# Kernel tuning notes

Hardware: AMD Instinct MI355X
Metric: run time of the kernel (lower is better)

## Reference

```python
import jax, jax.numpy as jnp
import numpy as np

EMB = 2048
HEADS = 16
HEAD = EMB // HEADS


def setup_inputs() -> dict:
    key = jax.random.key(0)
    ks = jax.random.split(key, 10)
    B, S = 4, 2048
    x = jax.random.normal(ks[0], (B, S, EMB), dtype=jnp.float32)
    # additive causal mask: 0 on/below diagonal, -inf above
    neg_inf = jnp.finfo(jnp.float32).min
    attn_mask = jnp.where(jnp.tril(jnp.ones((S, S), dtype=bool)), 0.0, neg_inf).astype(jnp.float32)
    scale = 1.0 / np.sqrt(EMB)  # xavier-ish init scale
    Wq = jax.random.normal(ks[1], (EMB, EMB), dtype=jnp.float32) * scale
    Wk = jax.random.normal(ks[2], (EMB, EMB), dtype=jnp.float32) * scale
    Wv = jax.random.normal(ks[3], (EMB, EMB), dtype=jnp.float32) * scale
    Wo = jax.random.normal(ks[4], (EMB, EMB), dtype=jnp.float32) * scale
    bq = jnp.zeros((EMB,), dtype=jnp.float32)
    bk = jnp.zeros((EMB,), dtype=jnp.float32)
    bv = jnp.zeros((EMB,), dtype=jnp.float32)
    bo = jnp.zeros((EMB,), dtype=jnp.float32)
    return {"x": x, "attn_mask": attn_mask, "Wq": Wq, "bq": bq, "Wk": Wk, "bk": bk,
            "Wv": Wv, "bv": bv, "Wo": Wo, "bo": bo}


def reference(x, attn_mask, Wq, bq, Wk, bk, Wv, bv, Wo, bo):
    B, S, E = x.shape
    # torch Linear: y = x @ W.T + b
    def proj(W, b):
        y = jnp.einsum('bse,fe->bsf', x, W) + b
        return y.reshape(B, S, HEADS, HEAD).transpose(0, 2, 1, 3)  # [B,H,S,D]
    q = proj(Wq, bq)
    k = proj(Wk, bk)
    v = proj(Wv, bv)
    scores = jnp.einsum('bhqd,bhkd->bhqk', q, k) / np.sqrt(HEAD)
    scores = scores + attn_mask  # broadcast [S,S] over [B,H,S,S]
    attn = jax.nn.softmax(scores, axis=-1)  # dropout p=0.0 -> identity
    ctx = jnp.einsum('bhqk,bhkd->bhqd', attn, v)
    ctx = ctx.transpose(0, 2, 1, 3).reshape(B, S, E)
    out = jnp.einsum('bse,fe->bsf', ctx, Wo) + bo
    return out
```

## Files before the change

kernel.cpp:

```cpp
#include <hip/hip_runtime.h>

#define BATCH 4
#define SEQ   2048
#define EMBD  2048
#define NHEAD 16
#define HEADD 128

#define GM (BATCH*SEQ)
#define GN EMBD
#define GK EMBD

typedef __attribute__((ext_vector_type(8))) short short8;
typedef __attribute__((ext_vector_type(4))) short s16x4;
typedef __attribute__((ext_vector_type(4))) float f32x4;

static __device__ __forceinline__ short f2bf(float f) {
  unsigned u = __builtin_bit_cast(unsigned, f);
  unsigned r = (u + 0x7fffu + ((u >> 16) & 1u)) >> 16;
  return (short)r;
}

static __device__ __forceinline__ unsigned cvt_pk_bf16(float lo, float hi) {
  unsigned r;
  asm("v_cvt_pk_bf16_f32 %0, %1, %2" : "=v"(r) : "v"(lo), "v"(hi));
  return r;
}

static __device__ __forceinline__ void glds16(const short* g, short* l) {
  __builtin_amdgcn_global_load_lds(
      (const __attribute__((address_space(1))) unsigned int*)g,
      (__attribute__((address_space(3))) unsigned int*)l, 16, 0, 0);
}

__global__ __launch_bounds__(256) void cvt_f32_bf16(
    const float* __restrict__ in, short* __restrict__ out, int n)
{
  int i = (blockIdx.x * 256 + threadIdx.x) * 8;
  if (i + 7 < n) {
    float4 a = *(const float4*)&in[i];
    float4 b = *(const float4*)&in[i + 4];
    short8 o;
    o[0] = f2bf(a.x); o[1] = f2bf(a.y); o[2] = f2bf(a.z); o[3] = f2bf(a.w);
    o[4] = f2bf(b.x); o[5] = f2bf(b.y); o[6] = f2bf(b.z); o[7] = f2bf(b.w);
    *(short8*)&out[i] = o;
  }
}

__global__ __launch_bounds__(256) void cvt_w4(
    const float* __restrict__ w0, const float* __restrict__ w1,
    const float* __restrict__ w2, const float* __restrict__ w3,
    short* __restrict__ o0, short* __restrict__ o1,
    short* __restrict__ o2, short* __restrict__ o3)
{
  const float* src = blockIdx.y == 0 ? w0 : blockIdx.y == 1 ? w1 : blockIdx.y == 2 ? w2 : w3;
  short*       dst = blockIdx.y == 0 ? o0 : blockIdx.y == 1 ? o1 : blockIdx.y == 2 ? o2 : o3;
  int i = (blockIdx.x * 256 + threadIdx.x) * 8;
  float4 a = *(const float4*)&src[i];
  float4 b = *(const float4*)&src[i + 4];
  short8 o;
  o[0] = f2bf(a.x); o[1] = f2bf(a.y); o[2] = f2bf(a.z); o[3] = f2bf(a.w);
  o[4] = f2bf(b.x); o[5] = f2bf(b.y); o[6] = f2bf(b.z); o[7] = f2bf(b.w);
  *(short8*)&dst[i] = o;
}

#define NKT (GK / 64)

template<bool F32OUT>
__global__ __launch_bounds__(512, 2) void gemm_bias_kernel(
    const short* __restrict__ A, const short* __restrict__ W,
    const float* __restrict__ bias, void* __restrict__ Cout)
{
  __shared__ short SH[2][2][2][128 * 64];

  const int tid  = threadIdx.x;
  const int lane = tid & 63;
  const int wv   = tid >> 6;
  const int quad = lane >> 4;
  const int l15  = lane & 15;
  const int rsw  = l15 & 7;

  const int bid = blockIdx.x;
  const int swz = (bid & 7) * 32 + (bid >> 3);
  const int n0 = (swz & 7) * 256;
  const int m0 = (swz >> 3) * 256;

  const int hA = wv >> 2;
  const int hB = (wv & 3) >> 1;
  const int bl = (wv & 1) * 64;

  int grow[2], gcol[2];
#pragma unroll
  for (int j = 0; j < 2; ++j) {
    int gi = j * 512 + tid;
    int row = gi >> 3, slot = gi & 7;
    grow[j] = row;
    gcol[j] = (slot ^ (row & 7)) * 8;
  }

#define STG(mat_, src_, rb_, kt_, h_) do {                                   \
    short* ld_ = &SH[(kt_) & 1][mat_][h_][0];                                \
    _Pragma("unroll")                                                        \
    for (int j = 0; j < 2; ++j)                                              \
      glds16(&src_[(size_t)((rb_) + (h_) * 128 + grow[j]) * GK +             \
                   (kt_) * 64 + gcol[j]],                                    \
             &ld_[(j * 512 + wv * 64) * 8]);                                 \
  } while (0)

#define ARD(mi_, ks_) (*(const short8*)&Abase[                               \
    (((mi_) * 16 + l15) * 8 + (((ks_) * 4 + quad) ^ rsw)) * 8])
#define BRD(ni_, ks_) (*(const short8*)&Bbase[                               \
    ((bl + (ni_) * 16 + l15) * 8 + (((ks_) * 4 + quad) ^ rsw)) * 8])

  const f32x4 zerov = {0.f, 0.f, 0.f, 0.f};
  f32x4 acc[8][4];
#pragma unroll
  for (int mi = 0; mi < 8; ++mi)
#pragma unroll
    for (int ni = 0; ni < 4; ++ni) acc[mi][ni] = zerov;

  STG(0, A, m0, 0, 0); STG(1, W, n0, 0, 0); STG(1, W, n0, 0, 1);
  STG(0, A, m0, 0, 1);
  STG(1, W, n0, 1, 0); STG(1, W, n0, 1, 1); STG(0, A, m0, 1, 0);
  asm volatile("s_waitcnt vmcnt(6)" ::: "memory");
  __builtin_amdgcn_sched_barrier(0);
  __builtin_amdgcn_s_barrier();

  for (int kt = 0; kt < NKT; ++kt) {
    const int d = kt & 1;
    const short* Abase = &SH[d][0][hA][0];
    const short* Bbase = &SH[d][1][hB][0];
    short8 afA[4][2], afB[4][2], bfA[2][2], bfB[2][2];

#pragma unroll
    for (int mi = 0; mi < 4; ++mi)
#pragma unroll
      for (int ks = 0; ks < 2; ++ks) afA[mi][ks] = ARD(mi, ks);
#pragma unroll
    for (int ni = 0; ni < 2; ++ni)
#pragma unroll
      for (int ks = 0; ks < 2; ++ks) bfA[ni][ks] = BRD(ni, ks);
    if (kt + 1 < NKT) STG(0, A, m0, kt + 1, 1);
    __builtin_amdgcn_sched_barrier(0);
    asm volatile("s_waitcnt lgkmcnt(8)" ::: "memory");
    __builtin_amdgcn_s_barrier();
    asm volatile("s_waitcnt lgkmcnt(0)" ::: "memory");
    __builtin_amdgcn_sched_barrier(0);
    __builtin_amdgcn_s_setprio(1);
#pragma unroll
    for (int mi = 0; mi < 4; ++mi)
#pragma unroll
      for (int ni = 0; ni < 2; ++ni)
#pragma unroll
        for (int ks = 0; ks < 2; ++ks)
          acc[mi][ni] = __builtin_amdgcn_mfma_f32_16x16x32_bf16(afA[mi][ks], bfA[ni][ks], acc[mi][ni], 0, 0, 0);
    __builtin_amdgcn_s_setprio(0);
    __builtin_amdgcn_sched_barrier(0);
    __builtin_amdgcn_s_barrier();

#pragma unroll
    for (int ni = 0; ni < 2; ++ni)
#pragma unroll
      for (int ks = 0; ks < 2; ++ks) bfB[ni][ks] = BRD(ni + 2, ks);
    __builtin_amdgcn_sched_barrier(0);
    __builtin_amdgcn_s_barrier();
    asm volatile("s_waitcnt lgkmcnt(0)" ::: "memory");
    __builtin_amdgcn_sched_barrier(0);
    __builtin_amdgcn_s_setprio(1);
#pragma unroll
    for (int mi = 0; mi < 4; ++mi)
#pragma unroll
      for (int ni = 0; ni < 2; ++ni)
#pragma unroll
        for (int ks = 0; ks < 2; ++ks)
          acc[mi][ni + 2] = __builtin_amdgcn_mfma_f32_16x16x32_bf16(afA[mi][ks], bfB[ni][ks], acc[mi][ni + 2], 0, 0, 0);
    __builtin_amdgcn_s_setprio(0);
    __builtin_amdgcn_sched_barrier(0);
    __builtin_amdgcn_s_barrier();

#pragma unroll
    for (int mi = 0; mi < 4; ++mi)
#pragma unroll
      for (int ks = 0; ks < 2; ++ks) afB[mi][ks] = ARD(mi + 4, ks);
    if (kt + 2 < NKT) STG(1, W, n0, kt + 2, 0);
    __builtin_amdgcn_sched_barrier(0);
    __builtin_amdgcn_s_barrier();
    asm volatile("s_waitcnt lgkmcnt(0)" ::: "memory");
    __builtin_amdgcn_sched_barrier(0);
    __builtin_amdgcn_s_setprio(1);
#pragma unroll
    for (int mi = 0; mi < 4; ++mi)
#pragma unroll
      for (int ni = 0; ni < 2; ++ni)
#pragma unroll
        for (int ks = 0; ks < 2; ++ks)
          acc[mi + 4][ni] = __builtin_amdgcn_mfma_f32_16x16x32_bf16(afB[mi][ks], bfA[ni][ks], acc[mi + 4][ni], 0, 0, 0);
    __builtin_amdgcn_s_setprio(0);
    __builtin_amdgcn_sched_barrier(0);
    __builtin_amdgcn_s_barrier();

    if (kt + 2 < NKT) { STG(1, W, n0, kt + 2, 1); STG(0, A, m0, kt + 2, 0); }
    if (kt + 2 < NKT)      asm volatile("s_waitcnt vmcnt(6)" ::: "memory");
    else if (kt + 1 < NKT) asm volatile("s_waitcnt vmcnt(0)" ::: "memory");
    __builtin_amdgcn_sched_barrier(0);
    __builtin_amdgcn_s_barrier();
    __builtin_amdgcn_sched_barrier(0);
    __builtin_amdgcn_s_setprio(1);
#pragma unroll
    for (int mi = 0; mi < 4; ++mi)
#pragma unroll
      for (int ni = 0; ni < 2; ++ni)
#pragma unroll
        for (int ks = 0; ks < 2; ++ks)
          acc[mi + 4][ni + 2] = __builtin_amdgcn_mfma_f32_16x16x32_bf16(afB[mi][ks], bfB[ni][ks], acc[mi + 4][ni + 2], 0, 0, 0);
    __builtin_amdgcn_s_setprio(0);
    __builtin_amdgcn_sched_barrier(0);
    __builtin_amdgcn_s_barrier();
  }
#undef STG
#undef ARD
#undef BRD

  const int wm0 = hA * 128;
  const int wn0 = (wv & 3) * 64;
#pragma unroll
  for (int mi = 0; mi < 8; ++mi) {
    int mg = m0 + wm0 + mi * 16 + quad * 4;
#pragma unroll
    for (int ni = 0; ni < 4; ++ni) {
      int ng = n0 + wn0 + ni * 16 + l15;
      float bv = bias[ng];
#pragma unroll
      for (int r = 0; r < 4; ++r) {
        float val = acc[mi][ni][r] + bv;
        if (F32OUT)
          ((float*)Cout)[(size_t)(mg + r) * GN + ng] = val;
        else
          ((short*)Cout)[(size_t)(mg + r) * GN + ng] = f2bf(val);
      }
    }
  }
}

__global__ __launch_bounds__(256) void transpose_v(
    const short* __restrict__ V, short* __restrict__ Vt)
{
  __shared__ short T[64][72];
  const int b  = blockIdx.z;
  const int n0 = blockIdx.x * 64;
  const int s0 = blockIdx.y * 64;
#pragma unroll
  for (int rr = 0; rr < 2; ++rr) {
    int c = rr * 256 + threadIdx.x;
    int srow = c >> 3;
    int ncol = (c & 7) << 3;
    *(short8*)&T[srow][ncol] = *(const short8*)&V[((size_t)b * SEQ + s0 + srow) * EMBD + n0 + ncol];
  }
  __syncthreads();
#pragma unroll
  for (int rr = 0; rr < 2; ++rr) {
    int c = rr * 256 + threadIdx.x;
    int nrow = c >> 3;
    int scol = (c & 7) << 3;
    short8 o;
#pragma unroll
    for (int j = 0; j < 8; ++j) o[j] = T[scol + j][nrow];
    *(short8*)&Vt[((size_t)b * EMBD + n0 + nrow) * SEQ + s0 + scol] = o;
  }
}

__global__ __launch_bounds__(256) void flash_attn(
    const short* __restrict__ Q, const short* __restrict__ K,
    const short* __restrict__ Vt, short* __restrict__ Ctx)
{
  __shared__ short Ksf[2][64 * 128];
  __shared__ short Vsf[2][128 * 64];
  __shared__ short Ps[4][16][72];

  const int bid  = blockIdx.x;
  const int slot = bid >> 3;
  const int grp  = ((bid & 7) << 3) | (slot >> 4);
  const int xq   = slot & 15;
  const int h = grp & 15, b = grp >> 4;

  const int tid = threadIdx.x, lane = tid & 63, wv = tid >> 6;
  const int quad = lane >> 4, l15 = lane & 15;

  const size_t bhq    = (size_t)b * SEQ * EMBD + (size_t)h * HEADD;
  const size_t vtbase = ((size_t)b * EMBD + (size_t)h * HEADD) * SEQ;
  const float SL2E = 0.08838834764831845f * 1.4426950408889634f;
  const float THRS = 8.0f / SL2E;
  const int NQT = SEQ / 64;

  int kco[4], koff[4], voff[4];
#pragma unroll
  for (int rr = 0; rr < 4; ++rr) {
    int c = rr * 4 + wv;
    int g = c * 64 + lane;
    kco[rr] = c * 512;
    { int row = g >> 4, col16 = (g & 15) ^ (row & 15);
      koff[rr] = row * EMBD + col16 * 8; }
    { int row = g >> 3, col8 = (g & 7) ^ (row & 7);
      voff[rr] = row * SEQ + col8 * 8; }
  }

#define STAGE(buf, kt_) do {                                                 \
    const short* kb_ = &K[bhq + (size_t)((kt_) * 64) * EMBD];                \
    const short* vb_ = &Vt[vtbase + (size_t)((kt_) * 64)];                   \
    _Pragma("unroll")                                                        \
    for (int rr = 0; rr < 4; ++rr) {                                         \
      glds16(&kb_[koff[rr]], &Ksf[buf][kco[rr]]);                            \
      glds16(&vb_[voff[rr]], &Vsf[buf][kco[rr]]);                            \
    }                                                                        \
  } while (0)

  const f32x4 zerov = {0.f, 0.f, 0.f, 0.f};

  for (int pass = 0; pass < 2; ++pass) {
    const int qt = pass ? (NQT - 1 - xq) : xq;
    const int qg    = qt * 64 + wv * 16 + l15;
    const int rowg0 = qt * 64 + wv * 16 + quad * 4;

    short8 qf[4];
#pragma unroll
    for (int ks = 0; ks < 4; ++ks)
      qf[ks] = *(const short8*)&Q[bhq + (size_t)qg * EMBD + ks * 32 + quad * 8];

    f32x4 oacc[8];
#pragma unroll
    for (int ni = 0; ni < 8; ++ni) oacc[ni] = zerov;
    float m_s = -INFINITY;
    float l_s = 0.f;

    __syncthreads();
    STAGE(0, 0);

    for (int kt = 0; kt <= qt; ++kt) {
      const int cur = kt & 1;
      __syncthreads();
      if (kt < qt) STAGE(cur ^ 1, kt + 1);

      f32x4 sA[4];
#pragma unroll
      for (int ni = 0; ni < 4; ++ni) sA[ni] = zerov;
#pragma unroll
      for (int ks = 0; ks < 4; ++ks)
#pragma unroll
        for (int ni = 0; ni < 4; ++ni) {
          int row = ni * 16 + l15;
          short8 kf = *(const short8*)&Ksf[cur][(row * 16 + ((ks * 4 + quad) ^ (row & 15))) * 8];
          sA[ni] = __builtin_amdgcn_mfma_f32_16x16x32_bf16(kf, qf[ks], sA[ni], 0, 0, 0);
        }

      if (kt == qt) {
        const int key00 = kt * 64;
#pragma unroll
        for (int ni = 0; ni < 4; ++ni)
#pragma unroll
          for (int r = 0; r < 4; ++r) {
            int keyg = key00 + ni * 16 + quad * 4 + r;
            if (keyg > qg) sA[ni][r] = -INFINITY;
          }
      }

      float mv = sA[0][0];
#pragma unroll
      for (int ni = 0; ni < 4; ++ni)
#pragma unroll
        for (int r = 0; r < 4; ++r)
          if (ni | r) mv = fmaxf(mv, sA[ni][r]);
      mv = fmaxf(mv, __shfl_xor(mv, 16, 64));
      mv = fmaxf(mv, __shfl_xor(mv, 32, 64));

      if (!__all(mv <= m_s + THRS)) {
        float mn = fmaxf(m_s, mv);
        float alpha = exp2f((m_s - mn) * SL2E);
        m_s = mn;
        l_s *= alpha;
        float al[4];
#pragma unroll
        for (int r = 0; r < 4; ++r) al[r] = __shfl(alpha, quad * 4 + r, 16);
#pragma unroll
        for (int ni = 0; ni < 8; ++ni)
#pragma unroll
          for (int r = 0; r < 4; ++r) oacc[ni][r] *= al[r];
      }

      float msl = m_s * SL2E;
      float sum = 0.f;
#pragma unroll
      for (int ni = 0; ni < 4; ++ni)
#pragma unroll
        for (int r = 0; r < 4; ++r) {
          float p = exp2f(sA[ni][r] * SL2E - msl);
          sA[ni][r] = p;
          sum += p;
        }
      sum += __shfl_xor(sum, 16, 64);
      sum += __shfl_xor(sum, 32, 64);
      l_s += sum;

#pragma unroll
      for (int ni = 0; ni < 4; ++ni) {
        uint2 pk;
        pk.x = cvt_pk_bf16(sA[ni][0], sA[ni][1]);
        pk.y = cvt_pk_bf16(sA[ni][2], sA[ni][3]);
        *(uint2*)&Ps[wv][l15][ni * 16 + quad * 4] = pk;
      }

      short8 pf[2];
#pragma unroll
      for (int ks = 0; ks < 2; ++ks)
        pf[ks] = *(const short8*)&Ps[wv][l15][ks * 32 + quad * 8];
#pragma unroll
      for (int ni = 0; ni < 8; ++ni)
#pragma unroll
        for (int ks = 0; ks < 2; ++ks) {
          int row = ni * 16 + l15;
          short8 vf = *(const short8*)&Vsf[cur][(row * 8 + ((ks * 4 + quad) ^ (row & 7))) * 8];
          oacc[ni] = __builtin_amdgcn_mfma_f32_16x16x32_bf16(pf[ks], vf, oacc[ni], 0, 0, 0);
        }
    }

    float linv = 1.0f / l_s;
    float iv[4];
#pragma unroll
    for (int r = 0; r < 4; ++r) iv[r] = __shfl(linv, quad * 4 + r, 16);
#pragma unroll
    for (int r = 0; r < 4; ++r)
#pragma unroll
      for (int ni = 0; ni < 8; ++ni)
        Ctx[bhq + (size_t)(rowg0 + r) * EMBD + ni * 16 + l15] = f2bf(oacc[ni][r] * iv[r]);
  }
#undef STAGE
}

extern "C" void kernel_launch(void* const* d_in, const int* in_sizes, int n_in,
                              void* d_out, int out_size, void* d_ws, size_t ws_size,
                              hipStream_t stream)
{
  const float* x  = (const float*)d_in[0];
  const float* Wq = (const float*)d_in[2];
  const float* bq = (const float*)d_in[3];
  const float* Wk = (const float*)d_in[4];
  const float* bk = (const float*)d_in[5];
  const float* Wv = (const float*)d_in[6];
  const float* bv = (const float*)d_in[7];
  const float* Wo = (const float*)d_in[8];
  const float* bo = (const float*)d_in[9];
  float* out = (float*)d_out;

  const size_t NE = (size_t)BATCH * SEQ * EMBD;
  const size_t NW = (size_t)EMBD * EMBD;
  short* xb  = (short*)d_ws;
  short* wqb = xb  + NE;
  short* wkb = wqb + NW;
  short* wvb = wkb + NW;
  short* wob = wvb + NW;
  short* q   = wob + NW;
  short* k   = q   + NE;
  short* v   = k   + NE;
  short* vt  = v   + NE;
  short* ctx = v;

  cvt_f32_bf16<<<NE / (256 * 8), 256, 0, stream>>>(x, xb, (int)NE);
  cvt_w4<<<dim3(NW / (256 * 8), 4), 256, 0, stream>>>(Wq, Wk, Wv, Wo, wqb, wkb, wvb, wob);

  dim3 gg((GM / 256) * (GN / 256));
  gemm_bias_kernel<false><<<gg, 512, 0, stream>>>(xb, wqb, bq, q);
  gemm_bias_kernel<false><<<gg, 512, 0, stream>>>(xb, wkb, bk, k);
  gemm_bias_kernel<false><<<gg, 512, 0, stream>>>(xb, wvb, bv, v);
  transpose_v<<<dim3(EMBD / 64, SEQ / 64, BATCH), 256, 0, stream>>>(v, vt);
  flash_attn<<<dim3((SEQ / 128) * NHEAD * BATCH), 256, 0, stream>>>(q, k, vt, ctx);
  gemm_bias_kernel<true><<<gg, 512, 0, stream>>>(ctx, wob, bo, out);
}
```

Before: 571.5 us.

## Enlarge flash-attention query tile to 128 rows with 8 waves per block

Raises the flash-attention block from 4 to 8 waves, each block now covering 128 query rows, so every staged K/V tile is reused by twice as many waves and the grid shrinks to 512 blocks with a new block-to-head mapping. It also swizzles the P scratch buffer in LDS to avoid bank conflicts, adds scheduling barriers around the async staging, and raises wave priority around the MFMA loops. The trade-offs are fewer blocks in the grid for load balancing, higher register pressure under the new launch bounds, and more diagonal-tile masking work per block.

```diff
diff --git a/kernel.cpp b/kernel.cpp
--- a/kernel.cpp
+++ b/kernel.cpp
@@ -268,18 +268,17 @@
   }
 }
 
-__global__ __launch_bounds__(256) void flash_attn(
+__global__ __launch_bounds__(512, 4) void flash_attn(
     const short* __restrict__ Q, const short* __restrict__ K,
     const short* __restrict__ Vt, short* __restrict__ Ctx)
 {
   __shared__ short Ksf[2][64 * 128];
   __shared__ short Vsf[2][128 * 64];
-  __shared__ short Ps[4][16][72];
-
-  const int bid  = blockIdx.x;
-  const int slot = bid >> 3;
-  const int grp  = ((bid & 7) << 3) | (slot >> 4);
-  const int xq   = slot & 15;
+  __shared__ short Ps[8][16 * 64];
+
+  const int bid = blockIdx.x;
+  const int grp = ((bid & 7) << 3) | (bid >> 6);
+  const int xq  = (bid >> 3) & 7;
   const int h = grp & 15, b = grp >> 4;
 
   const int tid = threadIdx.x, lane = tid & 63, wv = tid >> 6;
@@ -289,12 +288,12 @@
   const size_t vtbase = ((size_t)b * EMBD + (size_t)h * HEADD) * SEQ;
   const float SL2E = 0.08838834764831845f * 1.4426950408889634f;
   const float THRS = 8.0f / SL2E;
-  const int NQT = SEQ / 64;
-
-  int kco[4], koff[4], voff[4];
-#pragma unroll
-  for (int rr = 0; rr < 4; ++rr) {
-    int c = rr * 4 + wv;
+  const int NQT = SEQ / 128;
+
+  int kco[2], koff[2], voff[2];
+#pragma unroll
+  for (int rr = 0; rr < 2; ++rr) {
+    int c = rr * 8 + wv;
     int g = c * 64 + lane;
     kco[rr] = c * 512;
     { int row = g >> 4, col16 = (g & 15) ^ (row & 15);
@@ -307,7 +306,7 @@
     const short* kb_ = &K[bhq + (size_t)((kt_) * 64) * EMBD];                \
     const short* vb_ = &Vt[vtbase + (size_t)((kt_) * 64)];                   \
     _Pragma("unroll")                                                        \
-    for (int rr = 0; rr < 4; ++rr) {                                         \
+    for (int rr = 0; rr < 2; ++rr) {                                         \
       glds16(&kb_[koff[rr]], &Ksf[buf][kco[rr]]);                            \
       glds16(&vb_[voff[rr]], &Vsf[buf][kco[rr]]);                            \
     }                                                                        \
@@ -317,8 +316,9 @@
 
   for (int pass = 0; pass < 2; ++pass) {
     const int qt = pass ? (NQT - 1 - xq) : xq;
-    const int qg    = qt * 64 + wv * 16 + l15;
-    const int rowg0 = qt * 64 + wv * 16 + quad * 4;
+    const int qg    = qt * 128 + wv * 16 + l15;
+    const int rowg0 = qt * 128 + wv * 16 + quad * 4;
+    const int KTMAX = 2 * qt + 1;
 
     short8 qf[4];
 #pragma unroll
@@ -332,16 +332,21 @@
     float l_s = 0.f;
 
     __syncthreads();
+    __builtin_amdgcn_sched_barrier(0);
     STAGE(0, 0);
-
-    for (int kt = 0; kt <= qt; ++kt) {
+    __builtin_amdgcn_sched_barrier(0);
+
+    for (int kt = 0; kt <= KTMAX; ++kt) {
       const int cur = kt & 1;
       __syncthreads();
-      if (kt < qt) STAGE(cur ^ 1, kt + 1);
+      __builtin_amdgcn_sched_barrier(0);
+      if (kt < KTMAX) STAGE(cur ^ 1, kt + 1);
+      __builtin_amdgcn_sched_barrier(0);
 
       f32x4 sA[4];
 #pragma unroll
       for (int ni = 0; ni < 4; ++ni) sA[ni] = zerov;
+      __builtin_amdgcn_s_setprio(1);
 #pragma unroll
       for (int ks = 0; ks < 4; ++ks)
 #pragma unroll
@@ -350,8 +355,9 @@
           short8 kf = *(const short8*)&Ksf[cur][(row * 16 + ((ks * 4 + quad) ^ (row & 15))) * 8];
           sA[ni] = __builtin_amdgcn_mfma_f32_16x16x32_bf16(kf, qf[ks], sA[ni], 0, 0, 0);
         }
-
-      if (kt == qt) {
+      __builtin_amdgcn_s_setprio(0);
+
+      if (kt >= 2 * qt) {
         const int key00 = kt * 64;
 #pragma unroll
         for (int ni = 0; ni < 4; ++ni)
@@ -404,13 +410,16 @@
         uint2 pk;
         pk.x = cvt_pk_bf16(sA[ni][0], sA[ni][1]);
         pk.y = cvt_pk_bf16(sA[ni][2], sA[ni][3]);
-        *(uint2*)&Ps[wv][l15][ni * 16 + quad * 4] = pk;
+        int wg = (((ni * 2 + (quad >> 1)) ^ (l15 & 7)) << 3) + ((quad & 1) << 2);
+        *(uint2*)&Ps[wv][l15 * 64 + wg] = pk;
       }
 
       short8 pf[2];
 #pragma unroll
       for (int ks = 0; ks < 2; ++ks)
-        pf[ks] = *(const short8*)&Ps[wv][l15][ks * 32 + quad * 8];
+        pf[ks] = *(const short8*)&Ps[wv][l15 * 64 + (((ks * 4 + quad) ^ (l15 & 7)) << 3)];
+
+      __builtin_amdgcn_s_setprio(1);
 #pragma unroll
       for (int ni = 0; ni < 8; ++ni)
 #pragma unroll
@@ -419,6 +428,8 @@
           short8 vf = *(const short8*)&Vsf[cur][(row * 8 + ((ks * 4 + quad) ^ (row & 7))) * 8];
           oacc[ni] = __builtin_amdgcn_mfma_f32_16x16x32_bf16(pf[ks], vf, oacc[ni], 0, 0, 0);
         }
+      __builtin_amdgcn_s_setprio(0);
+      __builtin_amdgcn_sched_barrier(0);
     }
 
     float linv = 1.0f / l_s;
@@ -470,6 +481,6 @@
   gemm_bias_kernel<false><<<gg, 512, 0, stream>>>(xb, wkb, bk, k);
   gemm_bias_kernel<false><<<gg, 512, 0, stream>>>(xb, wvb, bv, v);
   transpose_v<<<dim3(EMBD / 64, SEQ / 64, BATCH), 256, 0, stream>>>(v, vt);
-  flash_attn<<<dim3((SEQ / 128) * NHEAD * BATCH), 256, 0, stream>>>(q, k, vt, ctx);
+  flash_attn<<<dim3(512), 512, 0, stream>>>(q, k, vt, ctx);
   gemm_bias_kernel<true><<<gg, 512, 0, stream>>>(ctx, wob, bo, out);
 }
```

Result: faster. 554.6 us (-3.0%).
